# Kernel optimization log

Measured on AMD Instinct MI355X. Metric: run time of the kernel, lower is better.

Reference implementation:

```python
import jax, jax.numpy as jnp
import numpy as np

D_MODEL = 768
N_HEADS = 12
D_HEAD = D_MODEL // N_HEADS


def setup_inputs() -> dict:
    key = jax.random.key(0)
    k_x, k_qw, k_qb, k_ow, k_ob = jax.random.split(key, 5)
    B, N = 2, 4096
    scale = 1.0 / np.sqrt(D_MODEL)
    return {
        "x": jax.random.normal(k_x, (B, N, D_MODEL), dtype=jnp.float32),
        # torch nn.Linear stores weight as [out_features, in_features]
        "qkv_w": jax.random.uniform(k_qw, (3 * D_MODEL, D_MODEL), jnp.float32, -scale, scale),
        "qkv_b": jax.random.uniform(k_qb, (3 * D_MODEL,), jnp.float32, -scale, scale),
        "out_w": jax.random.uniform(k_ow, (D_MODEL, D_MODEL), jnp.float32, -scale, scale),
        "out_b": jax.random.uniform(k_ob, (D_MODEL,), jnp.float32, -scale, scale),
    }


def reference(x, qkv_w, qkv_b, out_w, out_b):
    B, N, D = x.shape
    qkv = x @ qkv_w.T + qkv_b                                   # [B, N, 3D]
    qkv = qkv.reshape(B, N, 3, N_HEADS, D_HEAD)
    qkv = jnp.transpose(qkv, (2, 0, 3, 1, 4))                    # [3, B, H, N, d]
    q, k, v = qkv[0], qkv[1], qkv[2]
    scores = jnp.einsum("bhqd,bhkd->bhqk", q, k) / np.sqrt(D_HEAD)
    attn = jax.nn.softmax(scores, axis=-1)
    out = jnp.einsum("bhqk,bhkd->bhqd", attn, v)                 # [B, H, N, d]
    out = jnp.transpose(out, (0, 2, 1, 3)).reshape(B, N, D)
    return out @ out_w.T + out_b
```

## Files before the change

### kernel.cpp

```cpp
#include <hip/hip_runtime.h>
#include <cstdint>

#define SEQ 4096
#define NH 12
#define DH 64
#define DM 768
#define MT 8192
#define QKVN 2304

typedef __bf16 bf16;
typedef __attribute__((ext_vector_type(8))) __bf16 bf16x8;
typedef __attribute__((ext_vector_type(4))) __bf16 bf16x4;
typedef __attribute__((ext_vector_type(4))) float f32x4;
typedef __attribute__((ext_vector_type(16))) float f32x16;
typedef __attribute__((ext_vector_type(2))) int int2v;

__device__ __forceinline__ void async_ld16(const void* g, void* lds) {
  __builtin_amdgcn_global_load_lds(
      (__attribute__((address_space(1))) void*)(void*)g,
      (__attribute__((address_space(3))) void*)lds, 16, 0, 0);
}

__device__ __forceinline__ int pk_bf16(float a, float b) {
  union { int i; bf16 h[2]; } u;
  u.h[0] = (bf16)a; u.h[1] = (bf16)b;
  return u.i;
}

__device__ __forceinline__ float fast_exp2(float x) {
#if __has_builtin(__builtin_amdgcn_exp2f)
  return __builtin_amdgcn_exp2f(x);
#else
  return __expf(x * 0.6931471805599453f);
#endif
}

__device__ __forceinline__ void lane32_swap(int& a, int& b) {
#if __has_builtin(__builtin_amdgcn_permlane32_swap)
  int2v r = __builtin_amdgcn_permlane32_swap(a, b, false, false);
  a = r.x; b = r.y;
#else
  int hi = (threadIdx.x & 63) >> 5;
  int ra = __shfl_xor(a, 32, 64), rb = __shfl_xor(b, 32, 64);
  int na = hi ? rb : a;
  int nb = hi ? b : ra;
  a = na; b = nb;
#endif
}

#define NX4  (MT * DM / 4)
#define NW14 (QKVN * DM / 4)
#define NW24 (DM * DM / 4)
__global__ void cvt_all(const float* __restrict__ x, const float* __restrict__ w1,
                        const float* __restrict__ w2, bf16* __restrict__ xb,
                        bf16* __restrict__ wb1, bf16* __restrict__ wb2) {
  int i = blockIdx.x * blockDim.x + threadIdx.x;
  const float* src; bf16* dst; int j;
  if (i < NX4) { src = x; dst = xb; j = i; }
  else if (i < NX4 + NW14) { src = w1; dst = wb1; j = i - NX4; }
  else if (i < NX4 + NW14 + NW24) { src = w2; dst = wb2; j = i - NX4 - NW14; }
  else return;
  f32x4 v = ((const f32x4*)src)[j];
  bf16x4 o;
  o.x = (bf16)v.x; o.y = (bf16)v.y; o.z = (bf16)v.z; o.w = (bf16)v.w;
  ((bf16x4*)dst)[j] = o;
}

template<int MODE>
__global__ __launch_bounds__(256) void gemm_bt(
    const bf16* __restrict__ A, const bf16* __restrict__ Bw,
    const float* __restrict__ bias,
    bf16* __restrict__ outQ, bf16* __restrict__ outK, bf16* __restrict__ outVt,
    float* __restrict__ outF,
    int M, int N, int K)
{
  __shared__ bf16 sA[128 * 32];
  __shared__ bf16 sB[128 * 32];
  __shared__ bf16 sT[MODE == 0 ? 64 * 136 : 1];
  const int tid  = threadIdx.x;
  const int wave = tid >> 6;
  const int lane = tid & 63;
  const int l15  = lane & 15;
  const int quad = lane >> 4;
  const int m0 = blockIdx.y * 128;
  const int n0 = blockIdx.x * 128;
  const int rowbase = (wave >> 1) * 64;
  const int colbase = (wave & 1) * 64;

  f32x4 acc[4][4] = {};

  const int sr = lane >> 2;
  const int sc = (lane & 3) * 8;

  for (int kt = 0; kt < K; kt += 32) {
#pragma unroll
    for (int p = 0; p < 4; ++p) {
      int chunk = p * 4 + wave;
      int r = (chunk & 7) * 16 + sr;
      if (chunk < 8) {
        async_ld16(A + (size_t)(m0 + r) * K + kt + sc, &sA[(chunk & 7) * 512]);
      } else {
        async_ld16(Bw + (size_t)(n0 + r) * K + kt + sc, &sB[(chunk & 7) * 512]);
      }
    }
    __syncthreads();

    bf16x8 af[4], bfr[4];
#pragma unroll
    for (int rt = 0; rt < 4; ++rt)
      af[rt] = *(const bf16x8*)&sA[(rowbase + rt * 16 + l15) * 32 + quad * 8];
#pragma unroll
    for (int ct = 0; ct < 4; ++ct)
      bfr[ct] = *(const bf16x8*)&sB[(colbase + ct * 16 + l15) * 32 + quad * 8];
#pragma unroll
    for (int rt = 0; rt < 4; ++rt)
#pragma unroll
      for (int ct = 0; ct < 4; ++ct)
        acc[rt][ct] = __builtin_amdgcn_mfma_f32_16x16x32_bf16(af[rt], bfr[ct], acc[rt][ct], 0, 0, 0);
    __syncthreads();
  }

  if (MODE == 0) {
    const int g = n0 / DM;
    if (g < 2) {
      const float qscale = 0.125f * 1.4426950408889634f;
#pragma unroll
      for (int ct = 0; ct < 4; ++ct) {
        int j = n0 + colbase + ct * 16 + l15;
        float bj = bias[j];
        int f = j % DM;
        int h = f >> 6, d = f & 63;
#pragma unroll
        for (int rt = 0; rt < 4; ++rt) {
          int mrow = m0 + rowbase + rt * 16 + quad * 4;
#pragma unroll
          for (int r = 0; r < 4; ++r) {
            float v = acc[rt][ct][r] + bj;
            int m = mrow + r;
            int b = m >> 12, n = m & 4095;
            int bh = b * NH + h;
            if (g == 0) outQ[((size_t)bh * SEQ + n) * DH + d] = (bf16)(v * qscale);
            else        outK[((size_t)bh * SEQ + n) * DH + d] = (bf16)v;
          }
        }
      }
    } else {
      const int f0 = n0 - 2 * DM;
      const int b = m0 >> 12, n0m = m0 & 4095;
#pragma unroll
      for (int p = 0; p < 2; ++p) {
        __syncthreads();
        if (colbase == p * 64) {
#pragma unroll
          for (int ct = 0; ct < 4; ++ct) {
            int jl = ct * 16 + l15;
            float bj = bias[n0 + p * 64 + jl];
#pragma unroll
            for (int rt = 0; rt < 4; ++rt) {
              int ml = rowbase + rt * 16 + quad * 4;
#pragma unroll
              for (int r = 0; r < 4; ++r)
                sT[jl * 136 + ml + r] = (bf16)(acc[rt][ct][r] + bj);
            }
          }
        }
        __syncthreads();
#pragma unroll
        for (int p2 = 0; p2 < 4; ++p2) {
          int slot = p2 * 256 + tid;
          int jr = slot >> 4, mc = (slot & 15) * 8;
          int fj = f0 + p * 64 + jr;
          int h = fj >> 6, d = fj & 63;
          *(bf16x8*)&outVt[((size_t)(b * NH + h) * DH + d) * SEQ + n0m + mc] =
              *(const bf16x8*)&sT[jr * 136 + mc];
        }
      }
    }
  } else {
#pragma unroll
    for (int ct = 0; ct < 4; ++ct) {
      int j = n0 + colbase + ct * 16 + l15;
      float bj = bias[j];
#pragma unroll
      for (int rt = 0; rt < 4; ++rt) {
        int mrow = m0 + rowbase + rt * 16 + quad * 4;
#pragma unroll
        for (int r = 0; r < 4; ++r)
          outF[(size_t)(mrow + r) * N + j] = acc[rt][ct][r] + bj;
      }
    }
  }
}

__global__ __launch_bounds__(256) void flash_attn(
    const bf16* __restrict__ Q, const bf16* __restrict__ Kg,
    const bf16* __restrict__ Vt, bf16* __restrict__ Oout)
{
  __shared__ bf16 sK[2][64 * 64];
  __shared__ bf16 sV[2][64 * 64];
  __shared__ float sL[128];

  const int tid  = threadIdx.x;
  const int wave = tid >> 6;
  const int lane = tid & 63;
  const int l31  = lane & 31;
  const int hi   = lane >> 5;
  const int bh = blockIdx.y;
  const int q0w = blockIdx.x * 128 + wave * 32;

  const bf16* Qb = Q  + (size_t)bh * SEQ * DH;
  const bf16* Kb = Kg + (size_t)bh * SEQ * DH;
  const bf16* Vb = Vt + (size_t)bh * DH * SEQ;

  const int srow = lane >> 3;
  const int spg  = lane & 7;
  const int xk   = l31 & 7;

  bf16x8 qf[4];
#pragma unroll
  for (int dc = 0; dc < 4; ++dc)
    qf[dc] = *(const bf16x8*)&Qb[(size_t)(q0w + l31) * DH + dc * 16 + hi * 8];

  f32x16 o0 = {}, o1 = {};
  float lsum = 0.f;

#pragma unroll
  for (int j = 0; j < 2; ++j) {
    int r0 = wave * 16 + j * 8;
    int row = r0 + srow;
    int lg = spg ^ (row & 7);
    async_ld16(Kb + (size_t)row * DH + lg * 8, &sK[0][r0 * 64]);
    async_ld16(Vb + (size_t)row * SEQ + lg * 8, &sV[0][r0 * 64]);
  }
  __syncthreads();

  int p = 0;
  for (int kt = 0; kt < SEQ; kt += 64) {
    if (kt + 64 < SEQ) {
#pragma unroll
      for (int j = 0; j < 2; ++j) {
        int r0 = wave * 16 + j * 8;
        int row = r0 + srow;
        int lg = spg ^ (row & 7);
        async_ld16(Kb + (size_t)(kt + 64 + row) * DH + lg * 8, &sK[p ^ 1][r0 * 64]);
        async_ld16(Vb + (size_t)row * SEQ + kt + 64 + lg * 8, &sV[p ^ 1][r0 * 64]);
      }
    }

    const bf16* sKp = sK[p];
    const bf16* sVp = sV[p];
#pragma unroll
    for (int kb = 0; kb < 2; ++kb) {
      f32x16 s = {};
#pragma unroll
      for (int dc = 0; dc < 4; ++dc) {
        bf16x8 kf = *(const bf16x8*)&sKp[(kb * 32 + l31) * 64 + (((dc * 2 + hi) ^ xk) * 8)];
        s = __builtin_amdgcn_mfma_f32_32x32x16_bf16(kf, qf[dc], s, 0, 0, 0);
      }
      float pv[16]; float ls = 0.f;
#pragma unroll
      for (int i = 0; i < 16; ++i) { pv[i] = fast_exp2(s[i]); ls += pv[i]; }
      lsum += ls;
#pragma unroll
      for (int kc = 0; kc < 2; ++kc) {
        int g0a = pk_bf16(pv[8 * kc + 0], pv[8 * kc + 1]);
        int g0b = pk_bf16(pv[8 * kc + 2], pv[8 * kc + 3]);
        int g1a = pk_bf16(pv[8 * kc + 4], pv[8 * kc + 5]);
        int g1b = pk_bf16(pv[8 * kc + 6], pv[8 * kc + 7]);
        lane32_swap(g0a, g1a);
        lane32_swap(g0b, g1b);
        union { int i[4]; bf16x8 v; } Af;
        Af.i[0] = g0a; Af.i[1] = g0b; Af.i[2] = g1a; Af.i[3] = g1b;
        int vg = (kb * 4 + kc * 2 + hi) ^ xk;
        bf16x8 vf0 = *(const bf16x8*)&sVp[(l31)      * 64 + vg * 8];
        bf16x8 vf1 = *(const bf16x8*)&sVp[(32 + l31) * 64 + vg * 8];
        o0 = __builtin_amdgcn_mfma_f32_32x32x16_bf16(Af.v, vf0, o0, 0, 0, 0);
        o1 = __builtin_amdgcn_mfma_f32_32x32x16_bf16(Af.v, vf1, o1, 0, 0, 0);
      }
    }
    __syncthreads();
    p ^= 1;
  }

  float l0 = lsum + __shfl_xor(lsum, 32, 64);
  if (hi == 0) sL[wave * 32 + l31] = 1.0f / l0;
  __syncthreads();

  const int bg = bh / NH, h = bh % NH;
#pragma unroll
  for (int i = 0; i < 16; ++i) {
    int ql = 8 * (i >> 2) + (i & 3) + 4 * hi;
    float inv = sL[wave * 32 + ql];
    size_t base = (size_t)(bg * SEQ + q0w + ql) * DM + h * DH;
    Oout[base + l31]      = (bf16)(o0[i] * inv);
    Oout[base + 32 + l31] = (bf16)(o1[i] * inv);
  }
}

extern "C" void kernel_launch(void* const* d_in, const int* in_sizes, int n_in,
                              void* d_out, int out_size, void* d_ws, size_t ws_size,
                              hipStream_t stream) {
  const float* x     = (const float*)d_in[0];
  const float* qkv_w = (const float*)d_in[1];
  const float* qkv_b = (const float*)d_in[2];
  const float* out_w = (const float*)d_in[3];
  const float* out_b = (const float*)d_in[4];
  float* out = (float*)d_out;

  char* w = (char*)d_ws;
  bf16* xb    = (bf16*)w; w += (size_t)MT * DM * 2;
  bf16* wqkv  = (bf16*)w; w += (size_t)QKVN * DM * 2;
  bf16* wout  = (bf16*)w; w += (size_t)DM * DM * 2;
  bf16* Qw    = (bf16*)w; w += (size_t)MT * DM * 2;
  bf16* Kw    = (bf16*)w; w += (size_t)MT * DM * 2;
  bf16* Vtw   = (bf16*)w; w += (size_t)MT * DM * 2;
  bf16* attnV = (bf16*)w; w += (size_t)MT * DM * 2;

  const int tot4 = NX4 + NW14 + NW24;
  cvt_all<<<dim3((tot4 + 255) / 256), 256, 0, stream>>>(x, qkv_w, out_w, xb, wqkv, wout);

  gemm_bt<0><<<dim3(QKVN / 128, MT / 128), 256, 0, stream>>>(
      xb, wqkv, qkv_b, Qw, Kw, Vtw, nullptr, MT, QKVN, DM);

  flash_attn<<<dim3(SEQ / 128, 2 * NH), 256, 0, stream>>>(Qw, Kw, Vtw, attnV);

  gemm_bt<1><<<dim3(DM / 128, MT / 128), 256, 0, stream>>>(
      attnV, wout, out_b, nullptr, nullptr, nullptr, out, MT, DM, DM);
}
```

Measured before the change: 312.8 us.

## Compute softmax row sums via MFMA with ones vector and restructure attention loop

Replaces the per-lane VALU summation of exponentials and the LDS-based row-sum reduction with an extra MFMA against a ones vector, so the normaliser lands directly in the output layout. The double-buffered loop is manually unrolled by two with precomputed LDS offsets, and the LDS swizzle is changed to add a row-group term, likely to reduce bank conflicts. Pack conversion uses the hardware cvt_pk_bf16 builtin when available. The trade is one extra MFMA per PV step, and the sum now uses bf16-rounded probabilities, which matches the PV numerator.

```diff
diff --git a/kernel.cpp b/kernel.cpp
--- a/kernel.cpp
+++ b/kernel.cpp
@@ -11,6 +11,7 @@
 typedef __bf16 bf16;
 typedef __attribute__((ext_vector_type(8))) __bf16 bf16x8;
 typedef __attribute__((ext_vector_type(4))) __bf16 bf16x4;
+typedef __attribute__((ext_vector_type(2))) __bf16 bf16x2;
 typedef __attribute__((ext_vector_type(4))) float f32x4;
 typedef __attribute__((ext_vector_type(16))) float f32x16;
 typedef __attribute__((ext_vector_type(2))) int int2v;
@@ -22,9 +23,15 @@
 }
 
 __device__ __forceinline__ int pk_bf16(float a, float b) {
+#if __has_builtin(__builtin_amdgcn_cvt_pk_bf16_f32)
+  union { bf16x2 v; int i; } u;
+  u.v = __builtin_amdgcn_cvt_pk_bf16_f32(a, b);
+  return u.i;
+#else
   union { int i; bf16 h[2]; } u;
   u.h[0] = (bf16)a; u.h[1] = (bf16)b;
   return u.i;
+#endif
 }
 
 __device__ __forceinline__ float fast_exp2(float x) {
@@ -198,7 +205,6 @@
 {
   __shared__ bf16 sK[2][64 * 64];
   __shared__ bf16 sV[2][64 * 64];
-  __shared__ float sL[128];
 
   const int tid  = threadIdx.x;
   const int wave = tid >> 6;
@@ -214,83 +220,88 @@
 
   const int srow = lane >> 3;
   const int spg  = lane & 7;
-  const int xk   = l31 & 7;
 
   bf16x8 qf[4];
 #pragma unroll
   for (int dc = 0; dc < 4; ++dc)
     qf[dc] = *(const bf16x8*)&Qb[(size_t)(q0w + l31) * DH + dc * 16 + hi * 8];
 
-  f32x16 o0 = {}, o1 = {};
-  float lsum = 0.f;
-
-#pragma unroll
-  for (int j = 0; j < 2; ++j) {
-    int r0 = wave * 16 + j * 8;
-    int row = r0 + srow;
-    int lg = spg ^ (row & 7);
-    async_ld16(Kb + (size_t)row * DH + lg * 8, &sK[0][r0 * 64]);
-    async_ld16(Vb + (size_t)row * SEQ + lg * 8, &sV[0][r0 * 64]);
-  }
-  __syncthreads();
-
-  int p = 0;
-  for (int kt = 0; kt < SEQ; kt += 64) {
-    if (kt + 64 < SEQ) {
-#pragma unroll
-      for (int j = 0; j < 2; ++j) {
-        int r0 = wave * 16 + j * 8;
-        int row = r0 + srow;
-        int lg = spg ^ (row & 7);
-        async_ld16(Kb + (size_t)(kt + 64 + row) * DH + lg * 8, &sK[p ^ 1][r0 * 64]);
-        async_ld16(Vb + (size_t)row * SEQ + kt + 64 + lg * 8, &sV[p ^ 1][r0 * 64]);
-      }
-    }
-
-    const bf16* sKp = sK[p];
-    const bf16* sVp = sV[p];
+  bf16x8 ones1;
+#pragma unroll
+  for (int j = 0; j < 8; ++j) ones1[j] = (bf16)1.0f;
+
+  f32x16 o0 = {}, o1 = {}, o2 = {};
+  f32x16 zc = {};
+
+  const int keyk = (l31 & 7) ^ (((l31 >> 3) & 3) << 1);
+  int kOff[4], vOff[4];
+#pragma unroll
+  for (int dc = 0; dc < 4; ++dc)
+    kOff[dc] = l31 * 64 + (((dc * 2 + hi) ^ keyk) * 8);
+#pragma unroll
+  for (int k4 = 0; k4 < 4; ++k4)
+    vOff[k4] = l31 * 64 + (((k4 * 2 + hi) ^ keyk) * 8);
+
+  auto stage = [&](int kt, int buf) {
+#pragma unroll
+    for (int j = 0; j < 2; ++j) {
+      int r0 = wave * 16 + j * 8;
+      int row = r0 + srow;
+      int lg = spg ^ (row & 7) ^ (((row >> 3) & 3) << 1);
+      async_ld16(Kb + (size_t)(kt + row) * DH + lg * 8, &sK[buf][r0 * 64]);
+      async_ld16(Vb + (size_t)row * SEQ + kt + lg * 8, &sV[buf][r0 * 64]);
+    }
+  };
+
+  auto compute = [&](const bf16* sKp, const bf16* sVp) {
 #pragma unroll
     for (int kb = 0; kb < 2; ++kb) {
-      f32x16 s = {};
-#pragma unroll
-      for (int dc = 0; dc < 4; ++dc) {
-        bf16x8 kf = *(const bf16x8*)&sKp[(kb * 32 + l31) * 64 + (((dc * 2 + hi) ^ xk) * 8)];
+      f32x16 s;
+      {
+        bf16x8 kf = *(const bf16x8*)&sKp[kOff[0] + kb * 2048];
+        s = __builtin_amdgcn_mfma_f32_32x32x16_bf16(kf, qf[0], zc, 0, 0, 0);
+      }
+#pragma unroll
+      for (int dc = 1; dc < 4; ++dc) {
+        bf16x8 kf = *(const bf16x8*)&sKp[kOff[dc] + kb * 2048];
         s = __builtin_amdgcn_mfma_f32_32x32x16_bf16(kf, qf[dc], s, 0, 0, 0);
       }
-      float pv[16]; float ls = 0.f;
-#pragma unroll
-      for (int i = 0; i < 16; ++i) { pv[i] = fast_exp2(s[i]); ls += pv[i]; }
-      lsum += ls;
 #pragma unroll
       for (int kc = 0; kc < 2; ++kc) {
-        int g0a = pk_bf16(pv[8 * kc + 0], pv[8 * kc + 1]);
-        int g0b = pk_bf16(pv[8 * kc + 2], pv[8 * kc + 3]);
-        int g1a = pk_bf16(pv[8 * kc + 4], pv[8 * kc + 5]);
-        int g1b = pk_bf16(pv[8 * kc + 6], pv[8 * kc + 7]);
+        int g0a = pk_bf16(fast_exp2(s[8 * kc + 0]), fast_exp2(s[8 * kc + 1]));
+        int g0b = pk_bf16(fast_exp2(s[8 * kc + 2]), fast_exp2(s[8 * kc + 3]));
+        int g1a = pk_bf16(fast_exp2(s[8 * kc + 4]), fast_exp2(s[8 * kc + 5]));
+        int g1b = pk_bf16(fast_exp2(s[8 * kc + 6]), fast_exp2(s[8 * kc + 7]));
         lane32_swap(g0a, g1a);
         lane32_swap(g0b, g1b);
         union { int i[4]; bf16x8 v; } Af;
         Af.i[0] = g0a; Af.i[1] = g0b; Af.i[2] = g1a; Af.i[3] = g1b;
-        int vg = (kb * 4 + kc * 2 + hi) ^ xk;
-        bf16x8 vf0 = *(const bf16x8*)&sVp[(l31)      * 64 + vg * 8];
-        bf16x8 vf1 = *(const bf16x8*)&sVp[(32 + l31) * 64 + vg * 8];
+        bf16x8 vf0 = *(const bf16x8*)&sVp[vOff[kb * 2 + kc]];
+        bf16x8 vf1 = *(const bf16x8*)&sVp[vOff[kb * 2 + kc] + 2048];
         o0 = __builtin_amdgcn_mfma_f32_32x32x16_bf16(Af.v, vf0, o0, 0, 0, 0);
         o1 = __builtin_amdgcn_mfma_f32_32x32x16_bf16(Af.v, vf1, o1, 0, 0, 0);
-      }
-    }
+        o2 = __builtin_amdgcn_mfma_f32_32x32x16_bf16(Af.v, ones1, o2, 0, 0, 0);
+      }
+    }
+  };
+
+  stage(0, 0);
+  __syncthreads();
+
+  for (int kt = 0; kt < SEQ; kt += 128) {
+    if (kt + 64 < SEQ) stage(kt + 64, 1);
+    compute(sK[0], sV[0]);
     __syncthreads();
-    p ^= 1;
+    if (kt + 128 < SEQ) stage(kt + 128, 0);
+    compute(sK[1], sV[1]);
+    __syncthreads();
   }
-
-  float l0 = lsum + __shfl_xor(lsum, 32, 64);
-  if (hi == 0) sL[wave * 32 + l31] = 1.0f / l0;
-  __syncthreads();
 
   const int bg = bh / NH, h = bh % NH;
 #pragma unroll
   for (int i = 0; i < 16; ++i) {
     int ql = 8 * (i >> 2) + (i & 3) + 4 * hi;
-    float inv = sL[wave * 32 + ql];
+    float inv = 1.0f / o2[i];
     size_t base = (size_t)(bg * SEQ + q0w + ql) * DM + h * DH;
     Oout[base + l31]      = (bf16)(o0[i] * inv);
     Oout[base + 32 + l31] = (bf16)(o1[i] * inv);
```

Result: faster. 293.8 us (-6.1%).
